# Performance work log

Hardware: AMD Instinct MI355X
Metric: run time of the kernel (lower is better)

The kernel has to match this reference:

```python
import jax, jax.numpy as jnp
import numpy as np
from jax import lax

HEADS = 8
DIM_HEAD = 32
WINDOW = 64
RPROJ = 1  # number of global landmark tokens (dynamic projection rank)
DIM = 128
DEPTH = 2
H = W = 192
NEG = -1e9


def _ln(x, g, b, eps=1e-5):
    mu = jnp.mean(x, axis=-1, keepdims=True)
    var = jnp.mean((x - mu) ** 2, axis=-1, keepdims=True)
    return (x - mu) * lax.rsqrt(var + eps) * g + b


def _long_short_attn(x, ln_g, ln_b, Wq, Wkv, Wproj, lnl_g, lnl_b, lng_g, lng_b, Wo, bo):
    # x: (B, T, dim). PreNorm -> long-short attention (non-causal):
    # local windowed attention with +-1 window look-around + r global landmark
    # tokens built by a softmax dynamic projection over the sequence.
    B, T, _ = x.shape
    h, d, ws, r = HEADS, DIM_HEAD, WINDOW, RPROJ
    xn = _ln(x, ln_g, ln_b)
    q = (xn @ Wq).reshape(B, T, h, d).transpose(0, 2, 1, 3) * (d ** -0.5)
    kv = xn @ Wkv
    k = kv[..., : h * d].reshape(B, T, h, d).transpose(0, 2, 1, 3)
    v = kv[..., h * d:].reshape(B, T, h, d).transpose(0, 2, 1, 3)
    # global landmarks: softmax over sequence of dynamic projection of keys
    p = jax.nn.softmax(jnp.einsum('bhtd,dr->bhtr', k, Wproj), axis=2)
    gk = _ln(jnp.einsum('bhtr,bhtd->bhrd', p, k), lng_g, lng_b)  # (B,h,r,d)
    gv = jnp.einsum('bhtr,bhtd->bhrd', p, v)
    lk = _ln(k, lnl_g, lnl_b)
    # local windows with look-around of one window on each side
    w = T // ws
    lq = q.reshape(B, h, w, ws, d)
    lkw = lk.reshape(B, h, w, ws, d)
    lvw = v.reshape(B, h, w, ws, d)
    pad = ((0, 0), (0, 0), (1, 1), (0, 0), (0, 0))
    lkp = jnp.pad(lkw, pad)
    lvp = jnp.pad(lvw, pad)
    lk_la = jnp.concatenate([lkp[:, :, i:i + w] for i in range(3)], axis=3)  # (B,h,w,3ws,d)
    lv_la = jnp.concatenate([lvp[:, :, i:i + w] for i in range(3)], axis=3)
    sim_g = jnp.einsum('bhwid,bhrd->bhwir', lq, gk)       # (B,h,w,ws,r)
    sim_l = jnp.einsum('bhwid,bhwjd->bhwij', lq, lk_la)   # (B,h,w,ws,3ws)
    src = jnp.arange(w)[:, None] - 1 + jnp.arange(3)[None, :]
    valid = jnp.repeat((src >= 0) & (src < w), ws, axis=1)  # (w, 3ws)
    sim_l = jnp.where(valid[None, None, :, None, :], sim_l, NEG)
    attn = jax.nn.softmax(jnp.concatenate([sim_g, sim_l], axis=-1), axis=-1)
    out = (jnp.einsum('bhwir,bhrd->bhwid', attn[..., :r], gv)
           + jnp.einsum('bhwij,bhwjd->bhwid', attn[..., r:], lv_la))
    out = out.reshape(B, h, T, d).transpose(0, 2, 1, 3).reshape(B, T, h * d)
    return out @ Wo + bo


# axial permutations for dim_index=1 (from calculate_permutations(2, 1))
_PERMS = (((0, 3, 2, 1), (0, 3, 2, 1)),   # attend along H
          ((0, 2, 3, 1), (0, 3, 1, 2)))   # attend along W


def _forward(x, ln_g, ln_b, Wq, Wkv, Wproj, lnl_g, lnl_b, lng_g, lng_b, Wo, bo,
             cln_g, cln_b, conv1_w, conv1_b, conv2_w, conv2_b):
    dn = ('NCHW', 'OIHW', 'NCHW')
    for l in range(DEPTH):
        for a, (perm, inv) in enumerate(_PERMS):
            xa = jnp.transpose(x, perm)
            sh = xa.shape
            xa = xa.reshape(-1, sh[-2], sh[-1])
            xa = _long_short_attn(xa, ln_g[l, a], ln_b[l, a], Wq[l, a], Wkv[l, a],
                                  Wproj[l, a], lnl_g[l, a], lnl_b[l, a],
                                  lng_g[l, a], lng_b[l, a], Wo[l, a], bo[l, a])
            x = jnp.transpose(xa.reshape(sh), inv)
        # conv FFN: ChanLayerNorm -> Conv3x3 (dim->4dim) -> LeakyReLU -> Conv3x3 (4dim->dim)
        mu = jnp.mean(x, axis=1, keepdims=True)
        std = jnp.sqrt(jnp.mean((x - mu) ** 2, axis=1, keepdims=True))
        xn = (x - mu) / (std + 1e-5) * cln_g[l][None, :, None, None] + cln_b[l][None, :, None, None]
        hdd = lax.conv_general_dilated(xn, conv1_w[l], (1, 1), 'SAME', dimension_numbers=dn)
        hdd = hdd + conv1_b[l][None, :, None, None]
        hdd = jnp.where(hdd >= 0, hdd, 0.01 * hdd)  # LeakyReLU(0.01)
        x = lax.conv_general_dilated(hdd, conv2_w[l], (1, 1), 'SAME', dimension_numbers=dn)
        x = x + conv2_b[l][None, :, None, None]
    return x


def setup_inputs() -> dict:
    key = jax.random.key(0)
    ks = jax.random.split(key, 8)
    inner = HEADS * DIM_HEAD
    s = 0.05
    return {
        'x': jax.random.normal(ks[0], (1, DIM, H, W), jnp.float32),
        'ln_g': jnp.ones((DEPTH, 2, DIM), jnp.float32),
        'ln_b': jnp.zeros((DEPTH, 2, DIM), jnp.float32),
        'Wq': s * jax.random.normal(ks[1], (DEPTH, 2, DIM, inner), jnp.float32),
        'Wkv': s * jax.random.normal(ks[2], (DEPTH, 2, DIM, 2 * inner), jnp.float32),
        'Wproj': s * jax.random.normal(ks[3], (DEPTH, 2, DIM_HEAD, RPROJ), jnp.float32),
        'lnl_g': jnp.ones((DEPTH, 2, DIM_HEAD), jnp.float32),
        'lnl_b': jnp.zeros((DEPTH, 2, DIM_HEAD), jnp.float32),
        'lng_g': jnp.ones((DEPTH, 2, DIM_HEAD), jnp.float32),
        'lng_b': jnp.zeros((DEPTH, 2, DIM_HEAD), jnp.float32),
        'Wo': s * jax.random.normal(ks[4], (DEPTH, 2, inner, DIM), jnp.float32),
        'bo': jnp.zeros((DEPTH, 2, DIM), jnp.float32),
        'cln_g': jnp.ones((DEPTH, DIM), jnp.float32),
        'cln_b': jnp.zeros((DEPTH, DIM), jnp.float32),
        'conv1_w': s * jax.random.normal(ks[5], (DEPTH, 4 * DIM, DIM, 3, 3), jnp.float32),
        'conv1_b': jnp.zeros((DEPTH, 4 * DIM), jnp.float32),
        'conv2_w': s * jax.random.normal(ks[6], (DEPTH, DIM, 4 * DIM, 3, 3), jnp.float32),
        'conv2_b': jnp.zeros((DEPTH, DIM), jnp.float32),
    }


def reference(x, ln_g, ln_b, Wq, Wkv, Wproj, lnl_g, lnl_b, lng_g, lng_b, Wo, bo,
              cln_g, cln_b, conv1_w, conv1_b, conv2_w, conv2_b):
    return _forward(x, ln_g, ln_b, Wq, Wkv, Wproj, lnl_g, lnl_b, lng_g, lng_b,
                    Wo, bo, cln_g, cln_b, conv1_w, conv1_b, conv2_w, conv2_b)
```

## Files before the change

### kernel.cpp

```cpp
#include <hip/hip_runtime.h>
#include <math.h>

#define SP 36864
#define NC 128
#define PW 194
#define PSP (PW*PW)

typedef unsigned short u16;
typedef __attribute__((ext_vector_type(8))) short short8v;
typedef __attribute__((ext_vector_type(4))) float f32x4;

static __device__ __forceinline__ u16 bf16r(float f) {
    unsigned u = __builtin_bit_cast(unsigned, f);
    u += 0x7fffu + ((u >> 16) & 1u);
    return (u16)(u >> 16);
}
static __device__ __forceinline__ float b2f(u16 u) {
    unsigned v = ((unsigned)u) << 16;
    return __builtin_bit_cast(float, v);
}

#define GLOAD_LDS16(gp, lp)                                                     \
    __builtin_amdgcn_global_load_lds(                                           \
        (const __attribute__((address_space(1))) unsigned*)(gp),                \
        (__attribute__((address_space(3))) unsigned*)(lp), 16, 0, 0)

__global__ __launch_bounds__(256) void ln_rows_bf16_kernel(
    const float* __restrict__ X, const float* __restrict__ g,
    const float* __restrict__ b, u16* __restrict__ XN, int perm)
{
    int gid = blockIdx.x * 256 + threadIdx.x;
    int i0 = gid % 192, i1 = gid / 192;
    int sp = i1 * 192 + i0;
    int row = (perm == 0) ? (i0 * 192 + i1) : gid;
    float sum = 0.f, sq = 0.f;
    for (int c = 0; c < NC; ++c) {
        float v = X[(size_t)c * SP + sp];
        sum += v; sq += v * v;
    }
    float mu  = sum * (1.f / NC);
    float var = sq * (1.f / NC) - mu * mu;
    float rs  = rsqrtf(var + 1e-5f);
    u16* xr = XN + (size_t)row * NC;
    for (int c0 = 0; c0 < 16; ++c0) {
        unsigned pk[4];
        #pragma unroll
        for (int e = 0; e < 4; ++e) {
            int c = c0 * 8 + e * 2;
            float v0 = (X[(size_t)c * SP + sp]       - mu) * rs * g[c]     + b[c];
            float v1 = (X[(size_t)(c + 1) * SP + sp] - mu) * rs * g[c + 1] + b[c + 1];
            pk[e] = (unsigned)bf16r(v0) | ((unsigned)bf16r(v1) << 16);
        }
        *(uint4*)&xr[c0 * 8] = make_uint4(pk[0], pk[1], pk[2], pk[3]);
    }
}

__global__ __launch_bounds__(256) void repack_t_kernel(
    const float* __restrict__ in, u16* __restrict__ out, int K, int N)
{
    const float* ib = in + (size_t)blockIdx.y * K * N;
    u16* ob = out + (size_t)blockIdx.y * K * N;
    int o = blockIdx.x * 256 + threadIdx.x;
    if (o >= K * N) return;
    int n = o / K, k = o - n * K;
    ob[o] = bf16r(ib[(size_t)k * N + n]);
}

template<int KD, int MODE>
__global__ __launch_bounds__(256) void gemm_qkv_kernel(
    const u16* __restrict__ A, const u16* __restrict__ BT,
    u16* __restrict__ O0, u16* __restrict__ O1, float scale)
{
    __shared__ __align__(16) u16 As[128 * 64];
    __shared__ __align__(16) u16 Bs[64 * 64];
    const int m0 = blockIdx.y * 128, n0 = blockIdx.x * 64;
    const int tid = threadIdx.x, lane = tid & 63, wave = tid >> 6;
    const int lrow = lane & 15, g = lane >> 4;
    f32x4 acc[2][4];
    #pragma unroll
    for (int i = 0; i < 2; ++i)
        #pragma unroll
        for (int j = 0; j < 4; ++j) acc[i][j] = (f32x4){0.f, 0.f, 0.f, 0.f};

    for (int k0 = 0; k0 < KD; k0 += 64) {
        #pragma unroll
        for (int i = 0; i < 4; ++i) {
            int F = tid + i * 256;
            int row = F >> 3, wn = (F & 7) * 16;
            int sw = wn ^ ((row & 7) << 4);
            *(uint4*)&As[F * 8] = *(const uint4*)&A[(size_t)(m0 + row) * KD + k0 + (sw >> 1)];
        }
        #pragma unroll
        for (int i = 0; i < 2; ++i) {
            int F = tid + i * 256;
            int n = F >> 3, wn = (F & 7) * 16;
            int sw = wn ^ ((n & 7) << 4);
            *(uint4*)&Bs[F * 8] = *(const uint4*)&BT[(size_t)(n0 + n) * KD + k0 + (sw >> 1)];
        }
        __syncthreads();
        #pragma unroll
        for (int ks = 0; ks < 2; ++ks) {
            short8v af[2], bf[4];
            #pragma unroll
            for (int mt = 0; mt < 2; ++mt) {
                int row = wave * 32 + mt * 16 + lrow;
                int off = ((ks * 64 + g * 16) ^ ((row & 7) << 4)) >> 1;
                af[mt] = *(const short8v*)&As[row * 64 + off];
            }
            #pragma unroll
            for (int nt = 0; nt < 4; ++nt) {
                int n = nt * 16 + lrow;
                int off = ((ks * 64 + g * 16) ^ ((n & 7) << 4)) >> 1;
                bf[nt] = *(const short8v*)&Bs[n * 64 + off];
            }
            #pragma unroll
            for (int mt = 0; mt < 2; ++mt)
                #pragma unroll
                for (int nt = 0; nt < 4; ++nt)
                    acc[mt][nt] = __builtin_amdgcn_mfma_f32_16x16x32_bf16(
                        af[mt], bf[nt], acc[mt][nt], 0, 0, 0);
        }
        __syncthreads();
    }
    #pragma unroll
    for (int mt = 0; mt < 2; ++mt) {
        #pragma unroll
        for (int r = 0; r < 4; ++r) {
            int m = m0 + wave * 32 + mt * 16 + 4 * g + r;
            int bq = m / 192, t = m - bq * 192;
            #pragma unroll
            for (int nt = 0; nt < 4; ++nt) {
                int n = n0 + nt * 16 + lrow;
                float v = acc[mt][nt][r];
                if (MODE == 0) {
                    O0[((size_t)(bq * 8 + (n >> 5)) * 192 + t) * 32 + (n & 31)] = bf16r(v * scale);
                } else {
                    u16* dst = (n < 256) ? O0 : O1;
                    int nn = n & 255;
                    dst[((size_t)(bq * 8 + (nn >> 5)) * 192 + t) * 32 + (nn & 31)] = bf16r(v);
                }
            }
        }
    }
}

template<int PERM>
__global__ __launch_bounds__(256) void gemm_wo_kernel(
    const u16* __restrict__ A, const u16* __restrict__ BT,
    const float* __restrict__ bias, float* __restrict__ X)
{
    __shared__ __align__(16) char smem[64 * 132 * 4];
    u16* As = (u16*)smem;
    u16* Bs = (u16*)(smem + 16384);
    float (*et)[132] = (float (*)[132])smem;
    const int m0 = blockIdx.y * 128, n0 = blockIdx.x * 64;
    const int tid = threadIdx.x, lane = tid & 63, wave = tid >> 6;
    const int lrow = lane & 15, g = lane >> 4;
    f32x4 acc[2][4];
    #pragma unroll
    for (int i = 0; i < 2; ++i)
        #pragma unroll
        for (int j = 0; j < 4; ++j) acc[i][j] = (f32x4){0.f, 0.f, 0.f, 0.f};

    for (int k0 = 0; k0 < 256; k0 += 64) {
        #pragma unroll
        for (int i = 0; i < 4; ++i) {
            int F = tid + i * 256;
            int row = F >> 3, wn = (F & 7) * 16;
            int sw = wn ^ ((row & 7) << 4);
            int ml = m0 + row;
            int ra = (PERM == 0) ? ((ml % 192) * 192 + ml / 192) : ml;
            *(uint4*)&As[F * 8] = *(const uint4*)&A[(size_t)ra * 256 + k0 + (sw >> 1)];
        }
        #pragma unroll
        for (int i = 0; i < 2; ++i) {
            int F = tid + i * 256;
            int n = F >> 3, wn = (F & 7) * 16;
            int sw = wn ^ ((n & 7) << 4);
            *(uint4*)&Bs[F * 8] = *(const uint4*)&BT[(size_t)(n0 + n) * 256 + k0 + (sw >> 1)];
        }
        __syncthreads();
        #pragma unroll
        for (int ks = 0; ks < 2; ++ks) {
            short8v af[2], bf[4];
            #pragma unroll
            for (int mt = 0; mt < 2; ++mt) {
                int row = wave * 32 + mt * 16 + lrow;
                int off = ((ks * 64 + g * 16) ^ ((row & 7) << 4)) >> 1;
                af[mt] = *(const short8v*)&As[row * 64 + off];
            }
            #pragma unroll
            for (int nt = 0; nt < 4; ++nt) {
                int n = nt * 16 + lrow;
                int off = ((ks * 64 + g * 16) ^ ((n & 7) << 4)) >> 1;
                bf[nt] = *(const short8v*)&Bs[n * 64 + off];
            }
            #pragma unroll
            for (int mt = 0; mt < 2; ++mt)
                #pragma unroll
                for (int nt = 0; nt < 4; ++nt)
                    acc[mt][nt] = __builtin_amdgcn_mfma_f32_16x16x32_bf16(
                        af[mt], bf[nt], acc[mt][nt], 0, 0, 0);
        }
        __syncthreads();
    }
    __syncthreads();
    #pragma unroll
    for (int mt = 0; mt < 2; ++mt)
        #pragma unroll
        for (int nt = 0; nt < 4; ++nt)
            #pragma unroll
            for (int r = 0; r < 4; ++r)
                et[nt * 16 + lrow][wave * 32 + mt * 16 + 4 * g + r] = acc[mt][nt][r];
    __syncthreads();
    int nl = tid >> 2, mseg = (tid & 3) * 32;
    float bb = bias[n0 + nl];
    #pragma unroll
    for (int q = 0; q < 8; ++q) {
        float4 v;
        v.x = et[nl][mseg + q * 4 + 0] + bb;
        v.y = et[nl][mseg + q * 4 + 1] + bb;
        v.z = et[nl][mseg + q * 4 + 2] + bb;
        v.w = et[nl][mseg + q * 4 + 3] + bb;
        *(float4*)&X[(size_t)(n0 + nl) * SP + m0 + mseg + q * 4] = v;
    }
}

__global__ __launch_bounds__(256) void proj_lkln_kernel(
    u16* __restrict__ Kb, const u16* __restrict__ Vb,
    const float* __restrict__ wp, const float* __restrict__ lnl_g,
    const float* __restrict__ lnl_b, const float* __restrict__ lng_g,
    const float* __restrict__ lng_b, float* __restrict__ GK, float* __restrict__ GV)
{
    int bh = blockIdx.x, tid = threadIdx.x;
    size_t base = (size_t)bh * 6144;
    __shared__ float wps[32], sc[192], red[1], gkr[32];
    if (tid < 32) wps[tid] = wp[tid];
    __syncthreads();
    float kr[32]; float ksum = 0.f, ksq = 0.f;
    if (tid < 192) {
        float s = 0.f;
        #pragma unroll
        for (int p2 = 0; p2 < 4; ++p2) {
            short8v kv = *(const short8v*)&Kb[base + tid * 32 + p2 * 8];
            #pragma unroll
            for (int j = 0; j < 8; ++j) {
                float v = b2f((u16)kv[j]);
                kr[p2 * 8 + j] = v; s += v * wps[p2 * 8 + j];
                ksum += v; ksq += v * v;
            }
        }
        sc[tid] = s;
    }
    __syncthreads();
    if (tid < 64) {
        float m = fmaxf(fmaxf(sc[tid], sc[tid + 64]), sc[tid + 128]);
        for (int o = 32; o; o >>= 1) m = fmaxf(m, __shfl_xor(m, o));
        if (!tid) red[0] = m;
    }
    __syncthreads();
    float mx = red[0];
    if (tid < 192) sc[tid] = __expf(sc[tid] - mx);
    __syncthreads();
    if (tid < 64) {
        float s2 = sc[tid] + sc[tid + 64] + sc[tid + 128];
        for (int o = 32; o; o >>= 1) s2 += __shfl_xor(s2, o);
        if (!tid) red[0] = s2;
    }
    __syncthreads();
    float invs = 1.f / red[0];
    if (tid < 192) sc[tid] *= invs;
    __syncthreads();
    if (tid < 32) {
        float ka = 0.f, va = 0.f;
        for (int t = 0; t < 192; ++t) {
            float p = sc[t];
            ka += p * b2f(Kb[base + t * 32 + tid]);
            va += p * b2f(Vb[base + t * 32 + tid]);
        }
        gkr[tid] = ka;
        GV[(size_t)bh * 32 + tid] = va;
    }
    __syncthreads();
    if (tid < 32) {
        float mu = 0.f;
        for (int d = 0; d < 32; ++d) mu += gkr[d];
        mu *= (1.f / 32);
        float var = 0.f;
        for (int d = 0; d < 32; ++d) { float df = gkr[d] - mu; var += df * df; }
        var *= (1.f / 32);
        float rs = rsqrtf(var + 1e-5f);
        GK[(size_t)bh * 32 + tid] = (gkr[tid] - mu) * rs * lng_g[tid] + lng_b[tid];
    }
    __syncthreads();
    if (tid < 192) {
        float mu = ksum * (1.f / 32);
        float var = ksq * (1.f / 32) - mu * mu;
        float rs = rsqrtf(var + 1e-5f);
        #pragma unroll
        for (int p2 = 0; p2 < 4; ++p2) {
            unsigned pk[4];
            #pragma unroll
            for (int e = 0; e < 4; ++e) {
                int c = p2 * 8 + e * 2;
                float v0 = (kr[c]     - mu) * rs * lnl_g[c]     + lnl_b[c];
                float v1 = (kr[c + 1] - mu) * rs * lnl_g[c + 1] + lnl_b[c + 1];
                pk[e] = (unsigned)bf16r(v0) | ((unsigned)bf16r(v1) << 16);
            }
            *(uint4*)&Kb[base + tid * 32 + p2 * 8] = make_uint4(pk[0], pk[1], pk[2], pk[3]);
        }
    }
}

__global__ __launch_bounds__(256) void attn_mfma_kernel(
    const u16* __restrict__ Q, const u16* __restrict__ K, const u16* __restrict__ V,
    const float* __restrict__ GK, const float* __restrict__ GV, u16* __restrict__ AO)
{
    __shared__ __align__(16) u16 Ks[192][40];
    __shared__ __align__(16) u16 VTs[32][200];
    __shared__ __align__(16) u16 Ps[4][16][200];
    __shared__ float gks[32], gvs[32], sgs[192];
    const int bh = blockIdx.x, tid = threadIdx.x;
    const int lane = tid & 63, wave = tid >> 6, lrow = lane & 15, g = lane >> 4;
    const size_t base = (size_t)bh * 6144;

    if (tid < 32) { gks[tid] = GK[(size_t)bh * 32 + tid]; gvs[tid] = GV[(size_t)bh * 32 + tid]; }
    __syncthreads();
    #pragma unroll
    for (int i = 0; i < 3; ++i) {
        int f = tid + i * 256;
        int key = f >> 2, part = f & 3;
        *(uint4*)&Ks[key][part * 8] = *(const uint4*)&K[base + key * 32 + part * 8];
        uint4 vv = *(const uint4*)&V[base + key * 32 + part * 8];
        u16 tmp[8]; *(uint4*)tmp = vv;
        #pragma unroll
        for (int e = 0; e < 8; ++e) VTs[part * 8 + e][key] = tmp[e];
    }
    if (tid < 192) {
        float s = 0.f;
        #pragma unroll
        for (int p2 = 0; p2 < 4; ++p2) {
            short8v qv = *(const short8v*)&Q[base + tid * 32 + p2 * 8];
            #pragma unroll
            for (int j = 0; j < 8; ++j) s += b2f((u16)qv[j]) * gks[p2 * 8 + j];
        }
        sgs[tid] = s;
    }
    __syncthreads();

    for (int qi = 0; qi < 3; ++qi) {
        int qt = wave * 3 + qi;
        int q = qt * 16 + lrow;
        int ww = qt >> 2;
        int tlo = (ww == 0) ? 0 : (ww - 1) * 4;
        int thi = (ww == 2) ? 12 : (ww + 2) * 4;
        short8v qf = *(const short8v*)&Q[base + q * 32 + g * 8];
        f32x4 s[12];
        #pragma unroll
        for (int t = 0; t < 12; ++t) {
            if (t >= tlo && t < thi) {
                short8v kf = *(const short8v*)&Ks[t * 16 + lrow][g * 8];
                f32x4 z = (f32x4){0.f, 0.f, 0.f, 0.f};
                s[t] = __builtin_amdgcn_mfma_f32_16x16x32_bf16(kf, qf, z, 0, 0, 0);
            }
        }
        float sg = sgs[q];
        float m = sg;
        #pragma unroll
        for (int t = 0; t < 12; ++t) if (t >= tlo && t < thi)
            m = fmaxf(m, fmaxf(fmaxf(s[t][0], s[t][1]), fmaxf(s[t][2], s[t][3])));
        m = fmaxf(m, __shfl_xor(m, 16));
        m = fmaxf(m, __shfl_xor(m, 32));
        float l = 0.f;
        #pragma unroll
        for (int t = 0; t < 12; ++t) if (t >= tlo && t < thi) {
            #pragma unroll
            for (int r = 0; r < 4; ++r) { float p = __expf(s[t][r] - m); s[t][r] = p; l += p; }
        }
        l += __shfl_xor(l, 16);
        l += __shfl_xor(l, 32);
        float eg = __expf(sg - m);
        float inv = 1.f / (l + eg);
        float pgv = eg * inv;
        #pragma unroll
        for (int t = 0; t < 12; ++t) if (t >= tlo && t < thi) {
            unsigned u0 = (unsigned)bf16r(s[t][0] * inv) | ((unsigned)bf16r(s[t][1] * inv) << 16);
            unsigned u1 = (unsigned)bf16r(s[t][2] * inv) | ((unsigned)bf16r(s[t][3] * inv) << 16);
            *(uint2*)&Ps[wave][lrow][t * 16 + g * 4] = make_uint2(u0, u1);
        }
        f32x4 o[2] = {(f32x4){0.f,0.f,0.f,0.f}, (f32x4){0.f,0.f,0.f,0.f}};
        int slo = tlo >> 1, shi = thi >> 1;
        #pragma unroll
        for (int ss = 0; ss < 6; ++ss) if (ss >= slo && ss < shi) {
            short8v pa = *(const short8v*)&Ps[wave][lrow][ss * 32 + g * 8];
            #pragma unroll
            for (int dt = 0; dt < 2; ++dt) {
                short8v vb = *(const short8v*)&VTs[dt * 16 + lrow][ss * 32 + g * 8];
                o[dt] = __builtin_amdgcn_mfma_f32_16x16x32_bf16(pa, vb, o[dt], 0, 0, 0);
            }
        }
        int b = bh >> 3, h = bh & 7;
        #pragma unroll
        for (int r = 0; r < 4; ++r) {
            int qg = qt * 16 + 4 * g + r;
            float pg = __shfl(pgv, 4 * g + r);
            size_t rowbase = ((size_t)b * 192 + qg) * 256 + h * 32;
            #pragma unroll
            for (int dt = 0; dt < 2; ++dt) {
                int d = dt * 16 + lrow;
                AO[rowbase + d] = bf16r(o[dt][r] + pg * gvs[d]);
            }
        }
    }
}

__global__ __launch_bounds__(256) void chanln_bf16_kernel(
    const float* __restrict__ X, const float* __restrict__ g,
    const float* __restrict__ b, u16* __restrict__ out)
{
    int tid = threadIdx.x;
    int p = tid >> 2, qc = tid & 3;
    int pos = blockIdx.x * 64 + p;
    float xv[32];
    float sum = 0.f, sumsq = 0.f;
    #pragma unroll
    for (int c = 0; c < 32; ++c) {
        float v = X[(size_t)(qc * 32 + c) * SP + pos];
        xv[c] = v; sum += v; sumsq += v * v;
    }
    sum += __shfl_xor(sum, 1);  sum += __shfl_xor(sum, 2);
    sumsq += __shfl_xor(sumsq, 1); sumsq += __shfl_xor(sumsq, 2);
    float mu  = sum * (1.f / 128);
    float var = sumsq * (1.f / 128) - mu * mu;
    float inv = 1.f / (sqrtf(fmaxf(var, 0.f)) + 1e-5f);
    unsigned pk[16];
    #pragma unroll
    for (int c = 0; c < 16; ++c) {
        int c0 = qc * 32 + 2 * c;
        float v0 = (xv[2 * c]     - mu) * inv * g[c0]     + b[c0];
        float v1 = (xv[2 * c + 1] - mu) * inv * g[c0 + 1] + b[c0 + 1];
        pk[c] = (unsigned)bf16r(v0) | ((unsigned)bf16r(v1) << 16);
    }
    int y = pos / 192, x = pos - y * 192;
    uint4* dst = (uint4*)(out + ((size_t)(y + 1) * PW + x + 1) * 128 + qc * 32);
    #pragma unroll
    for (int q = 0; q < 4; ++q)
        dst[q] = make_uint4(pk[4*q], pk[4*q+1], pk[4*q+2], pk[4*q+3]);
}

__global__ __launch_bounds__(256) void wtrans_kernel(
    const float* __restrict__ w, u16* __restrict__ wT, int CO, int CI)
{
    const float* wb = w + (size_t)blockIdx.y * CO * CI * 9;
    u16* wTb = wT + (size_t)blockIdx.y * CO * CI * 9;
    int gidx = blockIdx.x * 256 + threadIdx.x;
    if (gidx >= CO * CI) return;
    const float* src = wb + (size_t)gidx * 9;
    #pragma unroll
    for (int k = 0; k < 9; ++k)
        wTb[(size_t)k * CO * CI + gidx] = bf16r(src[k]);
}

template<int CI, int CO, int NCO, int MODE>
__global__ __launch_bounds__(256) void conv_gemm_kernel(
    const u16* __restrict__ inP, const u16* __restrict__ wT,
    const float* __restrict__ bias, void* __restrict__ outp)
{
    __shared__ __align__(16) u16 smem_u[4 * 128 * 64];

    const int nwg = 288 * NCO;
    const int orig = blockIdx.x;
    const int wgid = (orig & 7) * (nwg >> 3) + (orig >> 3);
    const int co_t = wgid % NCO, sp_t = wgid / NCO;
    const int ty = sp_t / 3, tx = sp_t - ty * 3;
    const int y0 = ty * 2, x0 = tx * 64;
    const int co0 = co_t * 128;

    const int tid = threadIdx.x, lane = tid & 63, wave = tid >> 6;
    const int lrow = lane & 15, g = lane >> 4;
    const int wm = wave & 1, wn = wave >> 1;
    const int lane8 = lane >> 3, lanec = lane & 7;
    const int csrc = lanec ^ lane8;

    size_t aBase[4], bBase[4];
    #pragma unroll
    for (int i = 0; i < 4; ++i) {
        int rr = wave * 32 + i * 8 + lane8;
        int yl = rr >> 6, xl = rr & 63;
        aBase[i] = ((size_t)(y0 + yl) * PW + x0 + xl) * CI + csrc * 8;
        bBase[i] = (size_t)(co0 + rr) * CI + csrc * 8;
    }

    constexpr int CPK = CI / 64;
    constexpr int NK  = 9 * CPK;

    auto stage = [&](int buf, int kk) {
        int tap = kk / CPK, cc = kk - tap * CPK;
        int ky = tap / 3, kx = tap - ky * 3;
        size_t dA = (size_t)(ky * PW + kx) * CI + cc * 64;
        size_t dB = (size_t)tap * CO * CI + cc * 64;
        u16* Ad = smem_u + buf * 8192;
        u16* Bd = smem_u + 16384 + buf * 8192;
        #pragma unroll
        for (int i = 0; i < 4; ++i) {
            GLOAD_LDS16(inP + aBase[i] + dA, Ad + (wave * 32 + i * 8) * 64);
            GLOAD_LDS16(wT  + bBase[i] + dB, Bd + (wave * 32 + i * 8) * 64);
        }
    };

    f32x4 acc[4][4];
    #pragma unroll
    for (int i = 0; i < 4; ++i)
        #pragma unroll
        for (int j = 0; j < 4; ++j) acc[i][j] = (f32x4){0.f, 0.f, 0.f, 0.f};

    stage(0, 0);
    __syncthreads();
    int cur = 0;
    for (int kk = 0; kk < NK; ++kk) {
        if (kk + 1 < NK) stage(cur ^ 1, kk + 1);
        const u16* As = smem_u + cur * 8192;
        const u16* Bs = smem_u + 16384 + cur * 8192;
        #pragma unroll
        for (int ks = 0; ks < 2; ++ks) {
            short8v af[4], bf[4];
            #pragma unroll
            for (int fm = 0; fm < 4; ++fm) {
                int row = wm * 64 + fm * 16 + lrow;
                int ch = (ks * 4 + g) ^ (row & 7);
                af[fm] = *(const short8v*)&As[row * 64 + ch * 8];
            }
            #pragma unroll
            for (int fn = 0; fn < 4; ++fn) {
                int row = wn * 64 + fn * 16 + lrow;
                int ch = (ks * 4 + g) ^ (row & 7);
                bf[fn] = *(const short8v*)&Bs[row * 64 + ch * 8];
            }
            #pragma unroll
            for (int fm = 0; fm < 4; ++fm)
                #pragma unroll
                for (int fn = 0; fn < 4; ++fn)
                    acc[fm][fn] = __builtin_amdgcn_mfma_f32_16x16x32_bf16(
                        af[fm], bf[fn], acc[fm][fn], 0, 0, 0);
        }
        __syncthreads();
        cur ^= 1;
    }

    if (MODE == 0) {
        u16* out = (u16*)outp;
        #pragma unroll
        for (int fn = 0; fn < 4; ++fn) {
            int co = co0 + wn * 64 + fn * 16 + lrow;
            float bb = bias[co];
            #pragma unroll
            for (int fm = 0; fm < 4; ++fm) {
                #pragma unroll
                for (int r = 0; r < 4; ++r) {
                    int m = wm * 64 + fm * 16 + g * 4 + r;
                    int y = y0 + (m >> 6), x = x0 + (m & 63);
                    float v = acc[fm][fn][r] + bb;
                    v = (v >= 0.f) ? v : 0.01f * v;
                    out[((size_t)(y + 1) * PW + x + 1) * CO + co] = bf16r(v);
                }
            }
        }
    } else {
        float* out = (float*)outp;
        __syncthreads();
        float (*et)[17] = (float (*)[17])((char*)smem_u + wave * 4352);
        #pragma unroll
        for (int fn = 0; fn < 4; ++fn) {
            #pragma unroll
            for (int fm = 0; fm < 4; ++fm)
                #pragma unroll
                for (int r = 0; r < 4; ++r)
                    et[fm * 16 + g * 4 + r][lrow] = acc[fm][fn][r];
            __syncthreads();
            #pragma unroll
            for (int c2 = 0; c2 < 16; ++c2) {
                int co = co0 + wn * 64 + fn * 16 + c2;
                float v = et[lane][c2] + bias[co];
                out[(size_t)co * SP + (y0 + wm) * 192 + x0 + lane] = v;
            }
            __syncthreads();
        }
    }
}

extern "C" void kernel_launch(void* const* d_in, const int* in_sizes, int n_in,
                              void* d_out, int out_size, void* d_ws, size_t ws_size,
                              hipStream_t stream)
{
    const float* x_in    = (const float*)d_in[0];
    const float* ln_g    = (const float*)d_in[1];
    const float* ln_b    = (const float*)d_in[2];
    const float* Wq      = (const float*)d_in[3];
    const float* Wkv     = (const float*)d_in[4];
    const float* Wproj   = (const float*)d_in[5];
    const float* lnl_g   = (const float*)d_in[6];
    const float* lnl_b   = (const float*)d_in[7];
    const float* lng_g   = (const float*)d_in[8];
    const float* lng_b   = (const float*)d_in[9];
    const float* Wo      = (const float*)d_in[10];
    const float* bo      = (const float*)d_in[11];
    const float* cln_g   = (const float*)d_in[12];
    const float* cln_b   = (const float*)d_in[13];
    const float* conv1_w = (const float*)d_in[14];
    const float* conv1_b = (const float*)d_in[15];
    const float* conv2_w = (const float*)d_in[16];
    const float* conv2_b = (const float*)d_in[17];

    float* X = (float*)d_out;
    char* ws = (char*)d_ws;
    u16*   XN   = (u16*)(ws);
    u16*   AO   = (u16*)(ws + 9437184);
    u16*   Qb   = (u16*)(ws + 28311552);
    u16*   Kb   = (u16*)(ws + 47185920);
    u16*   Vb   = (u16*)(ws + 66060288);
    float* GK   = (float*)(ws + 84934656);
    float* GV   = (float*)(ws + 85131264);
    u16*   wqT  = (u16*)(ws + 85327872);
    u16*   wkvT = (u16*)(ws + 85590016);
    u16*   woT  = (u16*)(ws + 86114304);
    u16*   wT1  = (u16*)(ws + 86376448);
    u16*   wT2  = (u16*)(ws + 88735744);
    u16*   XNc16p = AO;
    u16*   HID16p = Qb;

    hipMemcpyAsync(X, x_in, (size_t)SP * NC * 4, hipMemcpyDeviceToDevice, stream);

    repack_t_kernel<<<dim3(128, 4), 256, 0, stream>>>(Wq, wqT, 128, 256);
    repack_t_kernel<<<dim3(256, 4), 256, 0, stream>>>(Wkv, wkvT, 128, 512);
    repack_t_kernel<<<dim3(128, 4), 256, 0, stream>>>(Wo, woT, 256, 128);
    wtrans_kernel<<<dim3(256, 2), 256, 0, stream>>>(conv1_w, wT1, 512, 128);
    wtrans_kernel<<<dim3(256, 2), 256, 0, stream>>>(conv2_w, wT2, 128, 512);

    const float qscale = 0.17677669529663687f;

    for (int l = 0; l < 2; ++l) {
        for (int a = 0; a < 2; ++a) {
            int la = l * 2 + a;
            ln_rows_bf16_kernel<<<144, 256, 0, stream>>>(
                X, ln_g + la * 128, ln_b + la * 128, XN, a);
            gemm_qkv_kernel<128, 0><<<dim3(4, 288), 256, 0, stream>>>(
                XN, wqT + (size_t)la * 32768, Qb, nullptr, qscale);
            gemm_qkv_kernel<128, 1><<<dim3(8, 288), 256, 0, stream>>>(
                XN, wkvT + (size_t)la * 65536, Kb, Vb, 1.f);
            proj_lkln_kernel<<<1536, 256, 0, stream>>>(
                Kb, Vb, Wproj + la * 32, lnl_g + la * 32, lnl_b + la * 32,
                lng_g + la * 32, lng_b + la * 32, GK, GV);
            attn_mfma_kernel<<<1536, 256, 0, stream>>>(Qb, Kb, Vb, GK, GV, AO);
            if (a == 0)
                gemm_wo_kernel<0><<<dim3(2, 288), 256, 0, stream>>>(
                    AO, woT + (size_t)la * 32768, bo + la * 128, X);
            else
                gemm_wo_kernel<1><<<dim3(2, 288), 256, 0, stream>>>(
                    AO, woT + (size_t)la * 32768, bo + la * 128, X);
        }
        hipMemsetAsync(XNc16p, 0, (size_t)PSP * 128 * 2, stream);
        hipMemsetAsync(HID16p, 0, (size_t)PSP * 512 * 2, stream);
        chanln_bf16_kernel<<<576, 256, 0, stream>>>(X, cln_g + l * 128, cln_b + l * 128, XNc16p);
        conv_gemm_kernel<128, 512, 4, 0><<<dim3(1152), 256, 0, stream>>>(
            XNc16p, wT1 + (size_t)l * 589824, conv1_b + l * 512, (void*)HID16p);
        conv_gemm_kernel<512, 128, 1, 1><<<dim3(288), 256, 0, stream>>>(
            HID16p, wT2 + (size_t)l * 589824, conv2_b + l * 128, (void*)X);
    }
}
```

Before: 1.107 ms.

## Parallelize landmark reduction and halve conv2 tile height for more workgroups

```diff
diff --git a/kernel.cpp b/kernel.cpp
--- a/kernel.cpp
+++ b/kernel.cpp
@@ -235,6 +235,7 @@
     int bh = blockIdx.x, tid = threadIdx.x;
     size_t base = (size_t)bh * 6144;
     __shared__ float wps[32], sc[192], red[1], gkr[32];
+    __shared__ float pkp[8][32], pvp[8][32];
     if (tid < 32) wps[tid] = wp[tid];
     __syncthreads();
     float kr[32]; float ksum = 0.f, ksq = 0.f;
@@ -271,15 +272,23 @@
     float invs = 1.f / red[0];
     if (tid < 192) sc[tid] *= invs;
     __syncthreads();
+    {
+        int d = tid & 31, grp = tid >> 5;
+        float ka = 0.f, va = 0.f;
+        for (int t = grp * 24; t < grp * 24 + 24; ++t) {
+            float p = sc[t];
+            ka += p * b2f(Kb[base + t * 32 + d]);
+            va += p * b2f(Vb[base + t * 32 + d]);
+        }
+        pkp[grp][d] = ka; pvp[grp][d] = va;
+    }
+    __syncthreads();
     if (tid < 32) {
-        float ka = 0.f, va = 0.f;
-        for (int t = 0; t < 192; ++t) {
-            float p = sc[t];
-            ka += p * b2f(Kb[base + t * 32 + tid]);
-            va += p * b2f(Vb[base + t * 32 + tid]);
-        }
-        gkr[tid] = ka;
-        GV[(size_t)bh * 32 + tid] = va;
+        float k8 = 0.f, v8 = 0.f;
+        #pragma unroll
+        for (int g2 = 0; g2 < 8; ++g2) { k8 += pkp[g2][tid]; v8 += pvp[g2][tid]; }
+        gkr[tid] = k8;
+        GV[(size_t)bh * 32 + tid] = v8;
     }
     __syncthreads();
     if (tid < 32) {
@@ -461,33 +470,40 @@
         wTb[(size_t)k * CO * CI + gidx] = bf16r(src[k]);
 }
 
-template<int CI, int CO, int NCO, int MODE>
+template<int CI, int CO, int NCO, int MY, int MODE>
 __global__ __launch_bounds__(256) void conv_gemm_kernel(
     const u16* __restrict__ inP, const u16* __restrict__ wT,
     const float* __restrict__ bias, void* __restrict__ outp)
 {
-    __shared__ __align__(16) u16 smem_u[4 * 128 * 64];
-
-    const int nwg = 288 * NCO;
+    constexpr int M     = MY * 64;
+    constexpr int AELEM = M * 64;
+    constexpr int NSP   = (MY == 2) ? 288 : 576;
+    constexpr int FN    = (MY == 2) ? 4 : 2;
+    __shared__ __align__(16) u16 smem_u[2 * AELEM + 2 * 128 * 64];
+
+    const int nwg = NSP * NCO;
     const int orig = blockIdx.x;
     const int wgid = (orig & 7) * (nwg >> 3) + (orig >> 3);
     const int co_t = wgid % NCO, sp_t = wgid / NCO;
     const int ty = sp_t / 3, tx = sp_t - ty * 3;
-    const int y0 = ty * 2, x0 = tx * 64;
+    const int y0 = ty * MY, x0 = tx * 64;
     const int co0 = co_t * 128;
 
     const int tid = threadIdx.x, lane = tid & 63, wave = tid >> 6;
     const int lrow = lane & 15, g = lane >> 4;
-    const int wm = wave & 1, wn = wave >> 1;
     const int lane8 = lane >> 3, lanec = lane & 7;
     const int csrc = lanec ^ lane8;
 
-    size_t aBase[4], bBase[4];
+    size_t aBase[MY * 2], bBase[4];
+    #pragma unroll
+    for (int i = 0; i < MY * 2; ++i) {
+        int rr = wave * (M / 4) + i * 8 + lane8;
+        int yl = rr >> 6, xl = rr & 63;
+        aBase[i] = ((size_t)(y0 + yl) * PW + x0 + xl) * CI + csrc * 8;
+    }
     #pragma unroll
     for (int i = 0; i < 4; ++i) {
         int rr = wave * 32 + i * 8 + lane8;
-        int yl = rr >> 6, xl = rr & 63;
-        aBase[i] = ((size_t)(y0 + yl) * PW + x0 + xl) * CI + csrc * 8;
         bBase[i] = (size_t)(co0 + rr) * CI + csrc * 8;
     }
 
@@ -499,65 +515,77 @@
         int ky = tap / 3, kx = tap - ky * 3;
         size_t dA = (size_t)(ky * PW + kx) * CI + cc * 64;
         size_t dB = (size_t)tap * CO * CI + cc * 64;
-        u16* Ad = smem_u + buf * 8192;
-        u16* Bd = smem_u + 16384 + buf * 8192;
-        #pragma unroll
-        for (int i = 0; i < 4; ++i) {
-            GLOAD_LDS16(inP + aBase[i] + dA, Ad + (wave * 32 + i * 8) * 64);
-            GLOAD_LDS16(wT  + bBase[i] + dB, Bd + (wave * 32 + i * 8) * 64);
-        }
+        u16* Ad = smem_u + buf * AELEM;
+        u16* Bd = smem_u + 2 * AELEM + buf * 8192;
+        #pragma unroll
+        for (int i = 0; i < MY * 2; ++i)
+            GLOAD_LDS16(inP + aBase[i] + dA, Ad + (wave * (M / 4) + i * 8) * 64);
+        #pragma unroll
+        for (int i = 0; i < 4; ++i)
+            GLOAD_LDS16(wT + bBase[i] + dB, Bd + (wave * 32 + i * 8) * 64);
     };
 
-    f32x4 acc[4][4];
+    const int aRowBase = (MY == 2) ? (wave & 1) * 64 : 0;
+    const int bRowBase = (MY == 2) ? (wave >> 1) * 64 : wave * 32;
+
+    f32x4 acc[4][FN];
     #pragma unroll
     for (int i = 0; i < 4; ++i)
         #pragma unroll
-        for (int j = 0; j < 4; ++j) acc[i][j] = (f32x4){0.f, 0.f, 0.f, 0.f};
+        for (int j = 0; j < FN; ++j) acc[i][j] = (f32x4){0.f, 0.f, 0.f, 0.f};
 
     stage(0, 0);
-    __syncthreads();
     int cur = 0;
     for (int kk = 0; kk < NK; ++kk) {
-        if (kk + 1 < NK) stage(cur ^ 1, kk + 1);
-        const u16* As = smem_u + cur * 8192;
-        const u16* Bs = smem_u + 16384 + cur * 8192;
+        if (kk + 1 < NK) {
+            stage(cur ^ 1, kk + 1);
+            if constexpr (MY == 2) asm volatile("s_waitcnt vmcnt(8)" ::: "memory");
+            else                   asm volatile("s_waitcnt vmcnt(6)" ::: "memory");
+        } else {
+            asm volatile("s_waitcnt vmcnt(0)" ::: "memory");
+        }
+        __builtin_amdgcn_s_barrier();
+        __builtin_amdgcn_sched_barrier(0);
+        const u16* As = smem_u + cur * AELEM;
+        const u16* Bs = smem_u + 2 * AELEM + cur * 8192;
         #pragma unroll
         for (int ks = 0; ks < 2; ++ks) {
-            short8v af[4], bf[4];
+            short8v af[4], bf[FN];
             #pragma unroll
             for (int fm = 0; fm < 4; ++fm) {
-                int row = wm * 64 + fm * 16 + lrow;
+                int row = aRowBase + fm * 16 + lrow;
                 int ch = (ks * 4 + g) ^ (row & 7);
                 af[fm] = *(const short8v*)&As[row * 64 + ch * 8];
             }
             #pragma unroll
-            for (int fn = 0; fn < 4; ++fn) {
-                int row = wn * 64 + fn * 16 + lrow;
+            for (int fn = 0; fn < FN; ++fn) {
+                int row = bRowBase + fn * 16 + lrow;
                 int ch = (ks * 4 + g) ^ (row & 7);
                 bf[fn] = *(const short8v*)&Bs[row * 64 + ch * 8];
             }
             #pragma unroll
             for (int fm = 0; fm < 4; ++fm)
                 #pragma unroll
-                for (int fn = 0; fn < 4; ++fn)
+                for (int fn = 0; fn < FN; ++fn)
                     acc[fm][fn] = __builtin_amdgcn_mfma_f32_16x16x32_bf16(
                         af[fm], bf[fn], acc[fm][fn], 0, 0, 0);
         }
-        __syncthreads();
+        __builtin_amdgcn_s_barrier();
         cur ^= 1;
     }
-
-    if (MODE == 0) {
+    __syncthreads();
+
+    if constexpr (MODE == 0) {
         u16* out = (u16*)outp;
         #pragma unroll
-        for (int fn = 0; fn < 4; ++fn) {
-            int co = co0 + wn * 64 + fn * 16 + lrow;
+        for (int fn = 0; fn < FN; ++fn) {
+            int co = co0 + bRowBase + fn * 16 + lrow;
             float bb = bias[co];
             #pragma unroll
             for (int fm = 0; fm < 4; ++fm) {
                 #pragma unroll
                 for (int r = 0; r < 4; ++r) {
-                    int m = wm * 64 + fm * 16 + g * 4 + r;
+                    int m = aRowBase + fm * 16 + g * 4 + r;
                     int y = y0 + (m >> 6), x = x0 + (m & 63);
                     float v = acc[fm][fn][r] + bb;
                     v = (v >= 0.f) ? v : 0.01f * v;
@@ -567,10 +595,9 @@
         }
     } else {
         float* out = (float*)outp;
-        __syncthreads();
         float (*et)[17] = (float (*)[17])((char*)smem_u + wave * 4352);
         #pragma unroll
-        for (int fn = 0; fn < 4; ++fn) {
+        for (int fn = 0; fn < FN; ++fn) {
             #pragma unroll
             for (int fm = 0; fm < 4; ++fm)
                 #pragma unroll
@@ -579,9 +606,9 @@
             __syncthreads();
             #pragma unroll
             for (int c2 = 0; c2 < 16; ++c2) {
-                int co = co0 + wn * 64 + fn * 16 + c2;
+                int co = co0 + bRowBase + fn * 16 + c2;
                 float v = et[lane][c2] + bias[co];
-                out[(size_t)co * SP + (y0 + wm) * 192 + x0 + lane] = v;
+                out[(size_t)co * SP + y0 * 192 + x0 + lane] = v;
             }
             __syncthreads();
         }
@@ -661,9 +688,9 @@
         hipMemsetAsync(XNc16p, 0, (size_t)PSP * 128 * 2, stream);
         hipMemsetAsync(HID16p, 0, (size_t)PSP * 512 * 2, stream);
         chanln_bf16_kernel<<<576, 256, 0, stream>>>(X, cln_g + l * 128, cln_b + l * 128, XNc16p);
-        conv_gemm_kernel<128, 512, 4, 0><<<dim3(1152), 256, 0, stream>>>(
+        conv_gemm_kernel<128, 512, 4, 2, 0><<<dim3(1152), 256, 0, stream>>>(
             XNc16p, wT1 + (size_t)l * 589824, conv1_b + l * 512, (void*)HID16p);
-        conv_gemm_kernel<512, 128, 1, 1><<<dim3(288), 256, 0, stream>>>(
+        conv_gemm_kernel<512, 128, 1, 1, 1><<<dim3(576), 256, 0, stream>>>(
             HID16p, wT2 + (size_t)l * 589824, conv2_b + l * 128, (void*)X);
     }
 }
```

New measurement: 950.9 us. 1.16x faster.
